# Kernel tuning notes

Hardware: AMD Instinct MI355X
Metric: run time of the kernel (lower is better)

## Reference

```python
import jax, jax.numpy as jnp
import numpy as np

DIM = 1024
HEADS = 16
DIM_HEAD = 64
INNER = HEADS * DIM_HEAD
EPS = 1e-5

def layernorm(x, g, b):
    mu = jnp.mean(x, axis=-1, keepdims=True)
    var = jnp.var(x, axis=-1, keepdims=True)
    return (x - mu) * jax.lax.rsqrt(var + EPS) * g + b

def setup_inputs() -> dict:
    key = jax.random.key(0)
    ks = jax.random.split(key, 9)
    b, t, n, m = 8, 8, 576, 64
    x = jax.random.normal(ks[0], (b, t, n, DIM), dtype=jnp.float32)
    latents = jax.random.normal(ks[1], (b, t, m, DIM), dtype=jnp.float32)
    att_mask = jax.random.randint(ks[2], (b, t, n), 0, 2, dtype=jnp.int32)
    s = 1.0 / np.sqrt(DIM)
    Wq = jax.random.normal(ks[3], (DIM, INNER), dtype=jnp.float32) * s
    Wkv = jax.random.normal(ks[4], (DIM, 2 * INNER), dtype=jnp.float32) * s
    Wo = jax.random.normal(ks[5], (INNER, DIM), dtype=jnp.float32) * (1.0 / np.sqrt(INNER))
    gm = jnp.ones((DIM,), jnp.float32); bm = jnp.zeros((DIM,), jnp.float32)
    gl = jnp.ones((DIM,), jnp.float32); bl = jnp.zeros((DIM,), jnp.float32)
    return {"x": x, "latents": latents, "att_mask": att_mask,
            "gm": gm, "bm": bm, "gl": gl, "bl": bl,
            "Wq": Wq, "Wkv": Wkv, "Wo": Wo}

def reference(x, latents, att_mask, gm, bm, gl, bl, Wq, Wkv, Wo):
    b, t, n, d = x.shape
    m = latents.shape[2]
    h, dh = HEADS, DIM_HEAD
    scale = dh ** -0.5

    xn = layernorm(x, gm, bm)
    ln = layernorm(latents, gl, bl)

    q = ln @ Wq                                  # b t m inner
    kv_input = jnp.concatenate((xn, ln), axis=-2)  # b t (n+m) d
    kv = kv_input @ Wkv                          # b t (n+m) 2*inner
    k, v = jnp.split(kv, 2, axis=-1)

    # b t s (h dh) -> b h t s dh
    def split_heads(a):
        bb, tt, ss, _ = a.shape
        return a.reshape(bb, tt, ss, h, dh).transpose(0, 3, 1, 2, 4)
    q = split_heads(q) * scale
    k = split_heads(k)
    v = split_heads(v)

    sim = jnp.einsum('bhtid,bhtjd->bhtij', q, k)   # b h t m (n+m)

    # mask: concat ones for latent KV positions; broadcast over heads and query dim
    full_mask = jnp.concatenate(
        [att_mask.astype(sim.dtype), jnp.ones((b, t, m), sim.dtype)], axis=2)  # b t (n+m)
    neg = jnp.finfo(sim.dtype).min
    bias = jnp.where(full_mask > 0, 0.0, neg)      # b t (n+m)
    sim = sim + bias[:, None, :, None, :]

    attn = jax.nn.softmax(sim, axis=-1)
    out = jnp.einsum('bhtij,bhtjd->bhtid', attn, v)  # b h t m dh
    out = out.transpose(0, 2, 3, 1, 4).reshape(b, t, m, h * dh)
    return out @ Wo
```

## Files before the change

### kernel.cpp

```cpp
#include <hip/hip_runtime.h>
#include <hip/hip_bf16.h>
#include <stdint.h>

#define NCTX 576
#define MLAT 64
#define SEQ 640
#define DMODEL 1024
#define NH 16
#define INNER_ 1024
#define KV_W 2048

typedef float f32x4 __attribute__((ext_vector_type(4)));
typedef __bf16 bf16x8 __attribute__((ext_vector_type(8)));
typedef unsigned short u16;
typedef unsigned int u32;
typedef unsigned long long u64;

typedef __attribute__((address_space(1))) u32 as1_u32;
typedef __attribute__((address_space(3))) u32 as3_u32;

__device__ __forceinline__ u16 f2bf(float f) {
    u32 u = __builtin_bit_cast(u32, f);
    u32 r = (u + 0x7fffu + ((u >> 16) & 1u)) >> 16;
    return (u16)r;
}

__device__ __forceinline__ int xcd_swizzle(int orig, int nwg) {
    int q = nwg >> 3, r = nwg & 7;
    int xcd = orig & 7, loc = orig >> 3;
    return (xcd < r ? xcd * (q + 1) : r * (q + 1) + (xcd - r) * q) + loc;
}

__global__ __launch_bounds__(256) void transpose_cast_all(const float* __restrict__ Wq,
                                                          const float* __restrict__ Wkv,
                                                          const float* __restrict__ Wo,
                                                          u16* __restrict__ WqT,
                                                          u16* __restrict__ WkvT,
                                                          u16* __restrict__ WoT) {
    __shared__ float tile[64][65];
    int id = blockIdx.x;
    const float* src; u16* dst; int N;
    if (id < 256)      { src = Wq;  dst = WqT;  N = 1024; }
    else if (id < 768) { src = Wkv; dst = WkvT; N = 2048; id -= 256; }
    else               { src = Wo;  dst = WoT;  N = 1024; id -= 768; }
    int nx = N >> 6;
    int n0 = (id % nx) * 64, k0 = (id / nx) * 64;
    int tid = threadIdx.x;
#pragma unroll
    for (int i = 0; i < 4; ++i) {
        int idx = i * 256 + tid;
        int kk = idx >> 4;
        int nn = (idx & 15) << 2;
        float4 v = *(const float4*)(src + (u64)(k0 + kk) * N + n0 + nn);
        tile[kk][nn] = v.x; tile[kk][nn + 1] = v.y; tile[kk][nn + 2] = v.z; tile[kk][nn + 3] = v.w;
    }
    __syncthreads();
#pragma unroll
    for (int i = 0; i < 4; ++i) {
        int idx = i * 256 + tid;
        int nn = idx >> 4;
        int kk = (idx & 15) << 2;
        ushort4 o;
        o.x = f2bf(tile[kk][nn]);     o.y = f2bf(tile[kk + 1][nn]);
        o.z = f2bf(tile[kk + 2][nn]); o.w = f2bf(tile[kk + 3][nn]);
        *(ushort4*)(dst + (u64)(n0 + nn) * 1024 + k0 + kk) = o;
    }
}

__global__ __launch_bounds__(256) void ln_cast(const float* __restrict__ x,
                                               const float* __restrict__ lat,
                                               const float* __restrict__ gm, const float* __restrict__ bm,
                                               const float* __restrict__ gl, const float* __restrict__ bl,
                                               u16* __restrict__ out, int nrows) {
    int w = threadIdx.x >> 6, lane = threadIdx.x & 63;
    int nw = gridDim.x * 4;
    for (int row = blockIdx.x * 4 + w; row < nrows; row += nw) {
        int bt = row / SEQ, s = row - bt * SEQ;
        const float *src, *g, *b;
        if (s < NCTX) { src = x + ((u64)bt * NCTX + s) * DMODEL; g = gm; b = bm; }
        else          { src = lat + ((u64)bt * MLAT + (s - NCTX)) * DMODEL; g = gl; b = bl; }
        float4 v[4];
        float sum = 0.f, sq = 0.f;
#pragma unroll
        for (int j = 0; j < 4; ++j) {
            v[j] = *(const float4*)(src + ((j * 64 + lane) << 2));
            sum += v[j].x + v[j].y + v[j].z + v[j].w;
            sq  += v[j].x * v[j].x + v[j].y * v[j].y + v[j].z * v[j].z + v[j].w * v[j].w;
        }
#pragma unroll
        for (int off = 1; off < 64; off <<= 1) {
            sum += __shfl_xor(sum, off, 64);
            sq  += __shfl_xor(sq, off, 64);
        }
        float mu = sum * (1.0f / DMODEL);
        float var = sq * (1.0f / DMODEL) - mu * mu;
        float rstd = rsqrtf(var + 1e-5f);
        u16* orow = out + (u64)row * DMODEL;
#pragma unroll
        for (int j = 0; j < 4; ++j) {
            float4 gv = *(const float4*)(g + ((j * 64 + lane) << 2));
            float4 bv = *(const float4*)(b + ((j * 64 + lane) << 2));
            ushort4 o;
            o.x = f2bf((v[j].x - mu) * rstd * gv.x + bv.x);
            o.y = f2bf((v[j].y - mu) * rstd * gv.y + bv.y);
            o.z = f2bf((v[j].z - mu) * rstd * gv.z + bv.z);
            o.w = f2bf((v[j].w - mu) * rstd * gv.w + bv.w);
            *(ushort4*)(orow + ((j * 64 + lane) << 2)) = o;
        }
    }
}

template <int WRITE_VT, typename OUT_T>
__global__ __launch_bounds__(256) void gemm_bf16(const u16* __restrict__ A,
                                                 const u16* __restrict__ Bt,
                                                 OUT_T* __restrict__ C, u16* __restrict__ vt,
                                                 int M, int ldc,
                                                 int rpgL2, long long gstride, float scale) {
    constexpr int K = 1024;
    __shared__ u16 As[128 * 32];
    __shared__ u16 Bs[128 * 32];
    int tid = threadIdx.x;
    int lane = tid & 63;
    int w = tid >> 6;
    int wm = w >> 1, wn = w & 1;
    int nwg = gridDim.x * gridDim.y;
    int wg = xcd_swizzle(blockIdx.y * gridDim.x + blockIdx.x, nwg);
    int m0 = (wg / gridDim.x) * 128;
    int n0 = (wg % gridDim.x) * 128;
    u32 rmask = (1u << rpgL2) - 1u;

    f32x4 acc[4][4] = {};

    for (int k0 = 0; k0 < K; k0 += 32) {
        __syncthreads();
#pragma unroll
        for (int i = 0; i < 2; ++i) {
            int t = i * 256 + tid;
            int r = t >> 2;
            int cg = t & 3;
            int col = (cg ^ ((r >> 1) & 3)) << 3;
            int grow = m0 + r; if (grow >= M) grow = M - 1;
            const u16* ga = A + (u64)(grow >> rpgL2) * (u64)gstride + (u64)(grow & rmask) * K + k0 + col;
            __builtin_amdgcn_global_load_lds((const as1_u32*)ga,
                (as3_u32*)(As + ((i * 256 + (w << 6)) << 3)), 16, 0, 0);
            const u16* gb = Bt + (u64)(n0 + r) * K + k0 + col;
            __builtin_amdgcn_global_load_lds((const as1_u32*)gb,
                (as3_u32*)(Bs + ((i * 256 + (w << 6)) << 3)), 16, 0, 0);
        }
        __syncthreads();
        bf16x8 a[4], b[4];
        int rl = lane & 15;
        int cgl = lane >> 4;
#pragma unroll
        for (int mi = 0; mi < 4; ++mi) {
            int r = wm * 64 + mi * 16 + rl;
            int c = (cgl ^ ((r >> 1) & 3)) << 3;
            a[mi] = *(const bf16x8*)(As + r * 32 + c);
        }
#pragma unroll
        for (int ni = 0; ni < 4; ++ni) {
            int r = wn * 64 + ni * 16 + rl;
            int c = (cgl ^ ((r >> 1) & 3)) << 3;
            b[ni] = *(const bf16x8*)(Bs + r * 32 + c);
        }
#pragma unroll
        for (int mi = 0; mi < 4; ++mi)
#pragma unroll
            for (int ni = 0; ni < 4; ++ni)
                acc[mi][ni] = __builtin_amdgcn_mfma_f32_16x16x32_bf16(a[mi], b[ni], acc[mi][ni], 0, 0, 0);
    }
    int rl = lane & 15, rg = lane >> 4;
    if constexpr (WRITE_VT) {
        int bt = m0 / SEQ;
        int s0 = m0 - bt * SEQ + wm * 64;
#pragma unroll
        for (int ni = 0; ni < 4; ++ni) {
            int vcol = n0 + wn * 64 + ni * 16 + rl;
            u16* vrow = vt + ((u64)bt * INNER_ + vcol) * SEQ;
#pragma unroll
            for (int mi = 0; mi < 4; ++mi) {
                int s = s0 + mi * 16 + rg * 4;
                ushort4 o;
                o.x = f2bf(acc[mi][ni][0] * scale);
                o.y = f2bf(acc[mi][ni][1] * scale);
                o.z = f2bf(acc[mi][ni][2] * scale);
                o.w = f2bf(acc[mi][ni][3] * scale);
                *(ushort4*)(vrow + s) = o;
            }
        }
    } else {
#pragma unroll
        for (int mi = 0; mi < 4; ++mi) {
#pragma unroll
            for (int r = 0; r < 4; ++r) {
                int grow = m0 + wm * 64 + mi * 16 + rg * 4 + r;
                if (grow < M) {
#pragma unroll
                    for (int ni = 0; ni < 4; ++ni) {
                        int gcol = n0 + wn * 64 + ni * 16 + rl;
                        float val = acc[mi][ni][r] * scale;
                        if constexpr (sizeof(OUT_T) == 2)
                            C[(u64)grow * ldc + gcol] = (OUT_T)f2bf(val);
                        else
                            C[(u64)grow * ldc + gcol] = val;
                    }
                }
            }
        }
    }
}

__global__ __launch_bounds__(256) void attn_kernel(const u16* __restrict__ qb,
                                                   const u16* __restrict__ kbuf,
                                                   const u16* __restrict__ vtb,
                                                   const int* __restrict__ mask,
                                                   u16* __restrict__ ob, int bt0) {
    int h = blockIdx.x;
    int btl = blockIdx.y;
    int tid = threadIdx.x, lane = tid & 63, w = tid >> 6;
    __shared__ u16 Ks[2][64 * 64];
    __shared__ u16 Vs[2][64 * 64];
    __shared__ u16 Ps[4][16 * 64];
    __shared__ float bias_s[2][64];
    int rl = lane & 15, cgl = lane >> 4;

    bf16x8 aq[2];
    {
        int qr = btl * MLAT + w * 16 + rl;
        const u16* qp = qb + (u64)qr * INNER_ + h * 64 + cgl * 8;
        aq[0] = *(const bf16x8*)(qp);
        aq[1] = *(const bf16x8*)(qp + 32);
    }
    f32x4 acc[4] = {};
    float mrow[4], lrow[4];
#pragma unroll
    for (int r = 0; r < 4; ++r) { mrow[r] = -1e30f; lrow[r] = 0.f; }

    const u16* kbase = kbuf + (u64)btl * SEQ * INNER_ + h * 64;
    const u16* vbase = vtb + ((u64)btl * INNER_ + h * 64) * SEQ;

    auto stage = [&](int c, int bf) {
#pragma unroll
        for (int i = 0; i < 2; ++i) {
            int t = i * 256 + tid;
            int r = t >> 3, cg = t & 7;
            int col = (cg ^ (r & 7)) << 3;
            __builtin_amdgcn_global_load_lds((const as1_u32*)(kbase + (u64)(c * 64 + r) * INNER_ + col),
                (as3_u32*)(&Ks[bf][0] + ((i * 256 + (w << 6)) << 3)), 16, 0, 0);
            __builtin_amdgcn_global_load_lds((const as1_u32*)(vbase + (u64)r * SEQ + c * 64 + col),
                (as3_u32*)(&Vs[bf][0] + ((i * 256 + (w << 6)) << 3)), 16, 0, 0);
        }
        if (tid < 64) {
            int pos = c * 64 + tid;
            bias_s[bf][tid] = (pos < NCTX) ? ((mask[(bt0 + btl) * NCTX + pos] > 0) ? 0.f : -1e30f) : 0.f;
        }
    };

    stage(0, 0);
    __syncthreads();

    for (int c = 0; c < SEQ / 64; ++c) {
        int bf = c & 1;
        if (c + 1 < SEQ / 64) stage(c + 1, bf ^ 1);

        f32x4 sf[4];
        __builtin_amdgcn_s_setprio(1);
#pragma unroll
        for (int ni = 0; ni < 4; ++ni) {
            f32x4 z = {};
#pragma unroll
            for (int kk = 0; kk < 2; ++kk) {
                int r = ni * 16 + rl;
                int g = (kk * 4 + cgl) ^ (r & 7);
                bf16x8 bk = *(const bf16x8*)(&Ks[bf][0] + r * 64 + g * 8);
                z = __builtin_amdgcn_mfma_f32_16x16x32_bf16(aq[kk], bk, z, 0, 0, 0);
            }
            float bias = bias_s[bf][ni * 16 + rl];
            z[0] += bias; z[1] += bias; z[2] += bias; z[3] += bias;
            sf[ni] = z;
        }
        __builtin_amdgcn_s_setprio(0);
        float alpha[4];
#pragma unroll
        for (int r = 0; r < 4; ++r) {
            float m = fmaxf(fmaxf(sf[0][r], sf[1][r]), fmaxf(sf[2][r], sf[3][r]));
            m = fmaxf(m, __shfl_xor(m, 1, 64));
            m = fmaxf(m, __shfl_xor(m, 2, 64));
            m = fmaxf(m, __shfl_xor(m, 4, 64));
            m = fmaxf(m, __shfl_xor(m, 8, 64));
            float mn = fmaxf(mrow[r], m);
            alpha[r] = __expf(mrow[r] - mn);
            mrow[r] = mn;
        }
#pragma unroll
        for (int ni = 0; ni < 4; ++ni)
#pragma unroll
            for (int r = 0; r < 4; ++r)
                sf[ni][r] = __expf(sf[ni][r] - mrow[r]);
#pragma unroll
        for (int r = 0; r < 4; ++r) {
            float s = sf[0][r] + sf[1][r] + sf[2][r] + sf[3][r];
            s += __shfl_xor(s, 1, 64);
            s += __shfl_xor(s, 2, 64);
            s += __shfl_xor(s, 4, 64);
            s += __shfl_xor(s, 8, 64);
            lrow[r] = lrow[r] * alpha[r] + s;
        }
        u16* pw = Ps[w];
#pragma unroll
        for (int ni = 0; ni < 4; ++ni) {
#pragma unroll
            for (int r = 0; r < 4; ++r) {
                int qrow = cgl * 4 + r;
                int kcol = ni * 16 + rl;
                int cs = (((kcol >> 3) ^ (qrow & 7)) << 3) + (kcol & 7);
                pw[qrow * 64 + cs] = f2bf(sf[ni][r]);
            }
        }
#pragma unroll
        for (int oi = 0; oi < 4; ++oi)
#pragma unroll
            for (int r = 0; r < 4; ++r)
                acc[oi][r] *= alpha[r];
        bf16x8 ap[2];
#pragma unroll
        for (int kk = 0; kk < 2; ++kk) {
            int cc = (((kk * 4 + cgl) ^ (rl & 7)) << 3);
            ap[kk] = *(const bf16x8*)(pw + rl * 64 + cc);
        }
        __builtin_amdgcn_s_setprio(1);
#pragma unroll
        for (int oi = 0; oi < 4; ++oi) {
#pragma unroll
            for (int kk = 0; kk < 2; ++kk) {
                int r = oi * 16 + rl;
                int g = (kk * 4 + cgl) ^ (r & 7);
                bf16x8 bv = *(const bf16x8*)(&Vs[bf][0] + r * 64 + g * 8);
                acc[oi] = __builtin_amdgcn_mfma_f32_16x16x32_bf16(ap[kk], bv, acc[oi], 0, 0, 0);
            }
        }
        __builtin_amdgcn_s_setprio(0);
        __syncthreads();
    }
#pragma unroll
    for (int r = 0; r < 4; ++r) {
        float inv = 1.0f / lrow[r];
        int qrow = btl * MLAT + w * 16 + cgl * 4 + r;
        u16* op = ob + (u64)qrow * INNER_ + h * 64;
#pragma unroll
        for (int oi = 0; oi < 4; ++oi)
            op[oi * 16 + rl] = f2bf(acc[oi][r] * inv);
    }
}

extern "C" void kernel_launch(void* const* d_in, const int* in_sizes, int n_in,
                              void* d_out, int out_size, void* d_ws, size_t ws_size,
                              hipStream_t stream) {
    const float* x    = (const float*)d_in[0];
    const float* lat  = (const float*)d_in[1];
    const int*   am   = (const int*)d_in[2];
    const float* gm   = (const float*)d_in[3];
    const float* bm   = (const float*)d_in[4];
    const float* gl   = (const float*)d_in[5];
    const float* bl   = (const float*)d_in[6];
    const float* Wq   = (const float*)d_in[7];
    const float* Wkv  = (const float*)d_in[8];
    const float* Wo   = (const float*)d_in[9];
    float* out = (float*)d_out;

    u16* WqT  = (u16*)d_ws;
    u16* WkvT = WqT + 1024 * 1024;
    u16* WoT  = WkvT + 2048 * 1024;
    u16* bufs = WoT + 1024 * 1024;

    size_t fixed = (size_t)(1024 * 1024 + 2048 * 1024 + 1024 * 1024) * 2;
    size_t perbt = (size_t)(SEQ * DMODEL + SEQ * INNER_ + INNER_ * SEQ + MLAT * INNER_ + MLAT * INNER_) * 2;
    int C = 64;
    while (C > 1 && fixed + (size_t)C * perbt > ws_size) C >>= 1;

    transpose_cast_all<<<1024, 256, 0, stream>>>(Wq, Wkv, Wo, WqT, WkvT, WoT);

    for (int bt0 = 0; bt0 < 64; bt0 += C) {
        u16* xn  = bufs;
        u16* kb  = xn + (size_t)C * SEQ * DMODEL;
        u16* vtp = kb + (size_t)C * SEQ * INNER_;
        u16* qbp = vtp + (size_t)C * INNER_ * SEQ;
        u16* ao  = qbp + (size_t)C * MLAT * INNER_;

        ln_cast<<<2048, 256, 0, stream>>>(x + (u64)bt0 * NCTX * DMODEL,
                                          lat + (u64)bt0 * MLAT * DMODEL,
                                          gm, bm, gl, bl, xn, C * SEQ);
        gemm_bf16<0, u16><<<dim3(INNER_ / 128, (C * SEQ) / 128), 256, 0, stream>>>(
            xn, WkvT, kb, nullptr, C * SEQ, INNER_, 30, 0, 1.0f);
        gemm_bf16<1, u16><<<dim3(INNER_ / 128, (C * SEQ) / 128), 256, 0, stream>>>(
            xn, WkvT + 1024 * 1024, (u16*)nullptr, vtp, C * SEQ, 0, 30, 0, 1.0f);
        gemm_bf16<0, u16><<<dim3(INNER_ / 128, (C * MLAT + 127) / 128), 256, 0, stream>>>(
            xn + NCTX * DMODEL, WqT, qbp, nullptr, C * MLAT, INNER_, 6, (long long)SEQ * DMODEL, 0.125f);
        attn_kernel<<<dim3(NH, C), 256, 0, stream>>>(qbp, kb, vtp, am, ao, bt0);
        gemm_bf16<0, float><<<dim3(DMODEL / 128, (C * MLAT + 127) / 128), 256, 0, stream>>>(
            ao, WoT, out + (u64)bt0 * MLAT * DMODEL, nullptr, C * MLAT, DMODEL, 30, 0, 1.0f);
    }
}
```

Before: 586.8 us.

## Compact unmasked KV positions and skip masked rows in LN, KV GEMM, attention

Adds a prefix-scan kernel that builds, per (b,t), a compacted list of unmasked context positions followed by the latent positions, plus a count. LayerNorm, the KV projection and attention then process only those valid rows, skipping GEMM tiles and attention chunks past the count, which removes roughly half the KV work for a random mask. It also merges the K and V projections into one GEMM launch over the full 2048-wide Wkv. The cost is an extra small kernel and data-dependent row indexing. Masked keys are dropped outright rather than given a very negative bias, which is mathematically equivalent.

```diff
diff --git a/kernel.cpp b/kernel.cpp
--- a/kernel.cpp
+++ b/kernel.cpp
@@ -29,6 +29,27 @@
     int q = nwg >> 3, r = nwg & 7;
     int xcd = orig & 7, loc = orig >> 3;
     return (xcd < r ? xcd * (q + 1) : r * (q + 1) + (xcd - r) * q) + loc;
+}
+
+__global__ __launch_bounds__(640) void build_idx(const int* __restrict__ mask,
+                                                 int* __restrict__ sidx,
+                                                 int* __restrict__ cnt,
+                                                 int* __restrict__ latst) {
+    int bt = blockIdx.x, tid = threadIdx.x;
+    __shared__ int ps[640];
+    int valid = (tid < NCTX) ? (mask[bt * NCTX + tid] > 0 ? 1 : 0) : 0;
+    ps[tid] = valid;
+    __syncthreads();
+    for (int off = 1; off < 640; off <<= 1) {
+        int v = (tid >= off) ? ps[tid - off] : 0;
+        __syncthreads();
+        ps[tid] += v;
+        __syncthreads();
+    }
+    int nc = ps[NCTX - 1];
+    if (valid) sidx[bt * SEQ + ps[tid] - 1] = tid;
+    if (tid < MLAT) sidx[bt * SEQ + nc + tid] = NCTX + tid;
+    if (tid == 0) { cnt[bt] = nc + MLAT; latst[bt] = nc; }
 }
 
 __global__ __launch_bounds__(256) void transpose_cast_all(const float* __restrict__ Wq,
@@ -71,14 +92,19 @@
                                                const float* __restrict__ lat,
                                                const float* __restrict__ gm, const float* __restrict__ bm,
                                                const float* __restrict__ gl, const float* __restrict__ bl,
-                                               u16* __restrict__ out, int nrows) {
+                                               u16* __restrict__ out,
+                                               const int* __restrict__ sidx, const int* __restrict__ cnt,
+                                               int bt0, int nrows) {
     int w = threadIdx.x >> 6, lane = threadIdx.x & 63;
     int nw = gridDim.x * 4;
     for (int row = blockIdx.x * 4 + w; row < nrows; row += nw) {
-        int bt = row / SEQ, s = row - bt * SEQ;
+        int btl = row / SEQ, jl = row - btl * SEQ;
+        int btg = bt0 + btl;
+        if (jl >= cnt[btg]) continue;
+        int sp = sidx[btg * SEQ + jl];
         const float *src, *g, *b;
-        if (s < NCTX) { src = x + ((u64)bt * NCTX + s) * DMODEL; g = gm; b = bm; }
-        else          { src = lat + ((u64)bt * MLAT + (s - NCTX)) * DMODEL; g = gl; b = bl; }
+        if (sp < NCTX) { src = x + ((u64)btl * NCTX + sp) * DMODEL; g = gm; b = bm; }
+        else           { src = lat + ((u64)btl * MLAT + (sp - NCTX)) * DMODEL; g = gl; b = bl; }
         float4 v[4];
         float sum = 0.f, sq = 0.f;
 #pragma unroll
@@ -110,12 +136,13 @@
     }
 }
 
-template <int WRITE_VT, typename OUT_T>
+template <int VT_SPLIT, typename OUT_T>
 __global__ __launch_bounds__(256) void gemm_bf16(const u16* __restrict__ A,
                                                  const u16* __restrict__ Bt,
                                                  OUT_T* __restrict__ C, u16* __restrict__ vt,
-                                                 int M, int ldc,
-                                                 int rpgL2, long long gstride, float scale) {
+                                                 int M, int ldc, float scale,
+                                                 const int* __restrict__ latstart,
+                                                 const int* __restrict__ cntp, int bt0) {
     constexpr int K = 1024;
     __shared__ u16 As[128 * 32];
     __shared__ u16 Bs[128 * 32];
@@ -127,7 +154,11 @@
     int wg = xcd_swizzle(blockIdx.y * gridDim.x + blockIdx.x, nwg);
     int m0 = (wg / gridDim.x) * 128;
     int n0 = (wg % gridDim.x) * 128;
-    u32 rmask = (1u << rpgL2) - 1u;
+
+    int btile = m0 / SEQ;
+    if (cntp) {
+        if (m0 - btile * SEQ >= cntp[bt0 + btile]) return;
+    }
 
     f32x4 acc[4][4] = {};
 
@@ -140,7 +171,14 @@
             int cg = t & 3;
             int col = (cg ^ ((r >> 1) & 3)) << 3;
             int grow = m0 + r; if (grow >= M) grow = M - 1;
-            const u16* ga = A + (u64)(grow >> rpgL2) * (u64)gstride + (u64)(grow & rmask) * K + k0 + col;
+            u64 row;
+            if (latstart) {
+                int lbt = grow >> 6;
+                row = (u64)lbt * SEQ + latstart[bt0 + lbt] + (grow & 63);
+            } else {
+                row = (u64)grow;
+            }
+            const u16* ga = A + row * K + k0 + col;
             __builtin_amdgcn_global_load_lds((const as1_u32*)ga,
                 (as3_u32*)(As + ((i * 256 + (w << 6)) << 3)), 16, 0, 0);
             const u16* gb = Bt + (u64)(n0 + r) * K + k0 + col;
@@ -170,13 +208,12 @@
                 acc[mi][ni] = __builtin_amdgcn_mfma_f32_16x16x32_bf16(a[mi], b[ni], acc[mi][ni], 0, 0, 0);
     }
     int rl = lane & 15, rg = lane >> 4;
-    if constexpr (WRITE_VT) {
-        int bt = m0 / SEQ;
-        int s0 = m0 - bt * SEQ + wm * 64;
+    if (VT_SPLIT && n0 >= INNER_) {
+        int s0 = m0 - btile * SEQ + wm * 64;
 #pragma unroll
         for (int ni = 0; ni < 4; ++ni) {
-            int vcol = n0 + wn * 64 + ni * 16 + rl;
-            u16* vrow = vt + ((u64)bt * INNER_ + vcol) * SEQ;
+            int vcol = (n0 - INNER_) + wn * 64 + ni * 16 + rl;
+            u16* vrow = vt + ((u64)btile * INNER_ + vcol) * SEQ;
 #pragma unroll
             for (int mi = 0; mi < 4; ++mi) {
                 int s = s0 + mi * 16 + rg * 4;
@@ -213,7 +250,7 @@
 __global__ __launch_bounds__(256) void attn_kernel(const u16* __restrict__ qb,
                                                    const u16* __restrict__ kbuf,
                                                    const u16* __restrict__ vtb,
-                                                   const int* __restrict__ mask,
+                                                   const int* __restrict__ cnt,
                                                    u16* __restrict__ ob, int bt0) {
     int h = blockIdx.x;
     int btl = blockIdx.y;
@@ -224,6 +261,9 @@
     __shared__ float bias_s[2][64];
     int rl = lane & 15, cgl = lane >> 4;
 
+    int cn = cnt[bt0 + btl];
+    int nch = (cn + 63) >> 6;
+
     bf16x8 aq[2];
     {
         int qr = btl * MLAT + w * 16 + rl;
@@ -252,16 +292,16 @@
         }
         if (tid < 64) {
             int pos = c * 64 + tid;
-            bias_s[bf][tid] = (pos < NCTX) ? ((mask[(bt0 + btl) * NCTX + pos] > 0) ? 0.f : -1e30f) : 0.f;
+            bias_s[bf][tid] = (pos < cn) ? 0.f : -1e30f;
         }
     };
 
     stage(0, 0);
     __syncthreads();
 
-    for (int c = 0; c < SEQ / 64; ++c) {
+    for (int c = 0; c < nch; ++c) {
         int bf = c & 1;
-        if (c + 1 < SEQ / 64) stage(c + 1, bf ^ 1);
+        if (c + 1 < nch) stage(c + 1, bf ^ 1);
 
         f32x4 sf[4];
         __builtin_amdgcn_s_setprio(1);
@@ -368,16 +408,20 @@
     const float* Wo   = (const float*)d_in[9];
     float* out = (float*)d_out;
 
-    u16* WqT  = (u16*)d_ws;
-    u16* WkvT = WqT + 1024 * 1024;
-    u16* WoT  = WkvT + 2048 * 1024;
-    u16* bufs = WoT + 1024 * 1024;
-
-    size_t fixed = (size_t)(1024 * 1024 + 2048 * 1024 + 1024 * 1024) * 2;
+    int* sidx  = (int*)d_ws;
+    int* cnt   = sidx + 64 * SEQ;
+    int* latst = cnt + 64;
+    u16* WqT   = (u16*)(latst + 64);
+    u16* WkvT  = WqT + 1024 * 1024;
+    u16* WoT   = WkvT + 2048 * 1024;
+    u16* bufs  = WoT + 1024 * 1024;
+
+    size_t fixed = (size_t)(64 * SEQ + 128) * 4 + (size_t)(1024 * 1024 + 2048 * 1024 + 1024 * 1024) * 2;
     size_t perbt = (size_t)(SEQ * DMODEL + SEQ * INNER_ + INNER_ * SEQ + MLAT * INNER_ + MLAT * INNER_) * 2;
     int C = 64;
     while (C > 1 && fixed + (size_t)C * perbt > ws_size) C >>= 1;
 
+    build_idx<<<64, 640, 0, stream>>>(am, sidx, cnt, latst);
     transpose_cast_all<<<1024, 256, 0, stream>>>(Wq, Wkv, Wo, WqT, WkvT, WoT);
 
     for (int bt0 = 0; bt0 < 64; bt0 += C) {
@@ -389,15 +433,13 @@
 
         ln_cast<<<2048, 256, 0, stream>>>(x + (u64)bt0 * NCTX * DMODEL,
                                           lat + (u64)bt0 * MLAT * DMODEL,
-                                          gm, bm, gl, bl, xn, C * SEQ);
-        gemm_bf16<0, u16><<<dim3(INNER_ / 128, (C * SEQ) / 128), 256, 0, stream>>>(
-            xn, WkvT, kb, nullptr, C * SEQ, INNER_, 30, 0, 1.0f);
-        gemm_bf16<1, u16><<<dim3(INNER_ / 128, (C * SEQ) / 128), 256, 0, stream>>>(
-            xn, WkvT + 1024 * 1024, (u16*)nullptr, vtp, C * SEQ, 0, 30, 0, 1.0f);
-        gemm_bf16<0, u16><<<dim3(INNER_ / 128, (C * MLAT + 127) / 128), 256, 0, stream>>>(
-            xn + NCTX * DMODEL, WqT, qbp, nullptr, C * MLAT, INNER_, 6, (long long)SEQ * DMODEL, 0.125f);
-        attn_kernel<<<dim3(NH, C), 256, 0, stream>>>(qbp, kb, vtp, am, ao, bt0);
-        gemm_bf16<0, float><<<dim3(DMODEL / 128, (C * MLAT + 127) / 128), 256, 0, stream>>>(
-            ao, WoT, out + (u64)bt0 * MLAT * DMODEL, nullptr, C * MLAT, DMODEL, 30, 0, 1.0f);
-    }
-}
+                                          gm, bm, gl, bl, xn, sidx, cnt, bt0, C * SEQ);
+        gemm_bf16<1, u16><<<dim3(KV_W / 128, (C * SEQ) / 128), 256, 0, stream>>>(
+            xn, WkvT, kb, vtp, C * SEQ, INNER_, 1.0f, nullptr, cnt, bt0);
+        gemm_bf16<0, u16><<<dim3(INNER_ / 128, (C * MLAT) / 128), 256, 0, stream>>>(
+            xn, WqT, qbp, nullptr, C * MLAT, INNER_, 0.125f, latst, nullptr, bt0);
+        attn_kernel<<<dim3(NH, C), 256, 0, stream>>>(qbp, kb, vtp, cnt, ao, bt0);
+        gemm_bf16<0, float><<<dim3(DMODEL / 128, (C * MLAT) / 128), 256, 0, stream>>>(
+            ao, WoT, out + (u64)bt0 * MLAT * DMODEL, nullptr, C * MLAT, DMODEL, 1.0f, nullptr, nullptr, 0);
+    }
+}
```

Result: faster. 478.0 us (-18.5%).
